# Optimization experiments

Hardware: AMD Instinct MI355X
Metric: run time of the kernel (lower is better)

The kernel has to match this reference:

```python
import jax, jax.numpy as jnp
import numpy as np

COMMISSION_RATIO = 0.0025
INTEREST_RATE = 0.00008
B, N = 4096, 8192


def setup_inputs() -> dict:
    key = jax.random.key(0)
    k1, k2 = jax.random.split(key)
    w = jax.random.uniform(k1, (B, 1, N), dtype=jnp.float32)
    w = w / jnp.sum(w, axis=-1, keepdims=True)  # portfolio weights sum to 1
    # price relatives close to 1 so log(reward) stays finite
    y = 1.0 + 0.02 * jax.random.normal(k2, (B, N, 1), dtype=jnp.float32)
    return {"w": w, "y": y}


def reference(w, y):
    # reward[b] = w[b] @ y[b]  -> [B,1,1]
    reward = jnp.einsum('bin,bnj->bij', w, y)
    # torch .view(B, 1, N) on contiguous [B, N, 1] == transpose here
    close_price = jnp.swapaxes(y, 1, 2)                     # [B,1,N]
    element_reward = w * close_price                        # [B,1,N]
    # interest: only negative elements contribute
    interest = jnp.sum(jnp.minimum(element_reward, 0.0), axis=2,
                       keepdims=True) * INTEREST_RATE       # [B,1,1]
    future_omega = element_reward / reward                  # [B,1,N]
    wt, wt1 = future_omega[:-1], w[1:]
    pure_pc = 1.0 - jnp.sum(jnp.abs(wt - wt1), axis=-1) * COMMISSION_RATIO  # [B-1,1]
    pure_pc = jnp.concatenate(
        [jnp.ones((1, 1), dtype=pure_pc.dtype), pure_pc], axis=0)  # [B,1]
    pure_pc = pure_pc[:, :, None]                           # [B,1,1]
    reward = reward * pure_pc + interest                    # [B,1,1]

    sr_reward = reward - 1.0
    SR = jnp.mean(sr_reward) / jnp.std(sr_reward, ddof=1)   # torch std is unbiased

    # max drawdown: cumprod of per-step changes, running max, relative dip
    pc = reward.reshape(-1)                                 # [B]
    pv = jnp.cumprod(pc)
    running_max = jax.lax.cummax(pv)
    MDD = jnp.max(1.0 - pv / running_max)

    portfolio_value = jnp.prod(reward, axis=0)              # [1,1]
    loss = -jnp.mean(jnp.log(reward))
    return loss, portfolio_value, SR, MDD
```

## Files before the change

### kernel.cpp

```cpp
#include <hip/hip_runtime.h>
#include <math.h>

#define B_DIM 4096
#define N_DIM 8192
#define K_ROWS 16
#define NBLK (B_DIM / K_ROWS)

__constant__ const float kCommission = 0.0025f;
__constant__ const float kInterest   = 8e-05f;

__global__ __launch_bounds__(256) void fused_reward_kernel(const float* __restrict__ w,
                                                           const float* __restrict__ y,
                                                           float* __restrict__ reward_out) {
    const int s    = blockIdx.x * K_ROWS;
    const int tid  = threadIdx.x;
    const int lane = tid & 63, wave = tid >> 6;
    __shared__ float red[2][4][3];

    const int rp = (s == 0) ? 0 : s - 1;
    {
        const float4* wb = (const float4*)(w + (size_t)rp * N_DIM);
        const float4* yb = (const float4*)(y + (size_t)rp * N_DIM);
        float4 wv[8], yv[8];
        #pragma unroll
        for (int j = 0; j < 8; ++j) wv[j] = wb[tid + 256 * j];
        #pragma unroll
        for (int j = 0; j < 8; ++j) yv[j] = yb[tid + 256 * j];
        float d = 0.f;
        float4 ep[8];
        #pragma unroll
        for (int j = 0; j < 8; ++j) {
            float4 ev;
            ev.x = wv[j].x * yv[j].x; ev.y = wv[j].y * yv[j].y;
            ev.z = wv[j].z * yv[j].z; ev.w = wv[j].w * yv[j].w;
            d += (ev.x + ev.y) + (ev.z + ev.w);
            ep[j] = ev;
        }
        (void)d; (void)ep;
    }

    float4 wv[8], yv[8];
    float4 e_prev[8];
    float  inv_dprev;

    {
        const float4* wb = (const float4*)(w + (size_t)rp * N_DIM);
        const float4* yb = (const float4*)(y + (size_t)rp * N_DIM);
        #pragma unroll
        for (int j = 0; j < 8; ++j) wv[j] = wb[tid + 256 * j];
        #pragma unroll
        for (int j = 0; j < 8; ++j) yv[j] = yb[tid + 256 * j];

        float d = 0.f;
        #pragma unroll
        for (int j = 0; j < 8; ++j) {
            float4 ev;
            ev.x = wv[j].x * yv[j].x; ev.y = wv[j].y * yv[j].y;
            ev.z = wv[j].z * yv[j].z; ev.w = wv[j].w * yv[j].w;
            d += (ev.x + ev.y) + (ev.z + ev.w);
            e_prev[j] = ev;
        }

        const float4* wc = (const float4*)(w + (size_t)s * N_DIM);
        const float4* yc = (const float4*)(y + (size_t)s * N_DIM);
        #pragma unroll
        for (int j = 0; j < 8; ++j) wv[j] = wc[tid + 256 * j];
        #pragma unroll
        for (int j = 0; j < 8; ++j) yv[j] = yc[tid + 256 * j];

        #pragma unroll
        for (int off = 32; off; off >>= 1) d += __shfl_down(d, off);
        if (lane == 0) red[0][wave][0] = d;
        __syncthreads();
        inv_dprev = 1.0f / ((red[0][0][0] + red[0][1][0]) + (red[0][2][0] + red[0][3][0]));
    }

    #pragma unroll 1
    for (int k = 0; k < K_ROWS; ++k) {
        const int r = s + k;

        float d = 0.f, it = 0.f, cm = 0.f;
        #pragma unroll
        for (int j = 0; j < 8; ++j) {
            float4 ev;
            ev.x = wv[j].x * yv[j].x; ev.y = wv[j].y * yv[j].y;
            ev.z = wv[j].z * yv[j].z; ev.w = wv[j].w * yv[j].w;
            d  += (ev.x + ev.y) + (ev.z + ev.w);
            it += (fminf(ev.x, 0.f) + fminf(ev.y, 0.f)) +
                  (fminf(ev.z, 0.f) + fminf(ev.w, 0.f));
            cm += (fabsf(fmaf(e_prev[j].x, inv_dprev, -wv[j].x)) +
                   fabsf(fmaf(e_prev[j].y, inv_dprev, -wv[j].y))) +
                  (fabsf(fmaf(e_prev[j].z, inv_dprev, -wv[j].z)) +
                   fabsf(fmaf(e_prev[j].w, inv_dprev, -wv[j].w)));
            e_prev[j] = ev;
        }

        if (k + 1 < K_ROWS) {
            const float4* wn = (const float4*)(w + (size_t)(r + 1) * N_DIM);
            const float4* yn = (const float4*)(y + (size_t)(r + 1) * N_DIM);
            #pragma unroll
            for (int j = 0; j < 8; ++j) wv[j] = wn[tid + 256 * j];
            #pragma unroll
            for (int j = 0; j < 8; ++j) yv[j] = yn[tid + 256 * j];
        }

        #pragma unroll
        for (int off = 32; off; off >>= 1) {
            d  += __shfl_down(d,  off);
            it += __shfl_down(it, off);
            cm += __shfl_down(cm, off);
        }
        const int pb = (k + 1) & 1;
        if (lane == 0) { red[pb][wave][0] = d; red[pb][wave][1] = it; red[pb][wave][2] = cm; }
        __syncthreads();
        const float dot_r = (red[pb][0][0] + red[pb][1][0]) + (red[pb][2][0] + red[pb][3][0]);
        const float int_r = ((red[pb][0][1] + red[pb][1][1]) + (red[pb][2][1] + red[pb][3][1])) * kInterest;
        const float comm  = (red[pb][0][2] + red[pb][1][2]) + (red[pb][2][2] + red[pb][3][2]);
        const float pc = (r == 0) ? 1.0f : fmaf(-comm, kCommission, 1.0f);
        if (tid == 0) reward_out[r] = dot_r * pc + int_r;
        inv_dprev = 1.0f / dot_r;
    }
}

__global__ __launch_bounds__(1024) void finalize_kernel(const float* __restrict__ reward,
                                                        float* __restrict__ out) {
    const int T = 1024, PER = B_DIM / T;
    const int tid = threadIdx.x;
    const int lane = tid & 63, wave = tid >> 6;

    float r[PER], lc[PER];
    float csum = 0.f;
    #pragma unroll
    for (int j = 0; j < PER; ++j) {
        r[j] = reward[tid * PER + j];
        csum += logf(r[j]);
        lc[j] = csum;
    }

    float v = csum;
    #pragma unroll
    for (int off = 1; off < 64; off <<= 1) {
        float t = __shfl_up(v, off);
        if (lane >= off) v += t;
    }
    __shared__ float wsum[16];
    __shared__ float woff[17];
    if (lane == 63) wsum[wave] = v;
    __syncthreads();
    if (tid == 0) {
        float acc = 0.f;
        for (int i = 0; i < 16; ++i) { woff[i] = acc; acc += wsum[i]; }
        woff[16] = acc;
    }
    __syncthreads();
    float ev = __shfl_up(v, 1);
    if (lane == 0) ev = 0.f;
    const float excl = woff[wave] + ev;
    float S[PER];
    #pragma unroll
    for (int j = 0; j < PER; ++j) S[j] = excl + lc[j];
    const float total_logs = woff[16];

    float rm = -INFINITY;
    float cmax[PER];
    #pragma unroll
    for (int j = 0; j < PER; ++j) { rm = fmaxf(rm, S[j]); cmax[j] = rm; }
    float mv = rm;
    #pragma unroll
    for (int off = 1; off < 64; off <<= 1) {
        float t = __shfl_up(mv, off);
        if (lane >= off) mv = fmaxf(mv, t);
    }
    __shared__ float wmax[16];
    __shared__ float wmoff[16];
    if (lane == 63) wmax[wave] = mv;
    __syncthreads();
    if (tid == 0) {
        float acc = -INFINITY;
        for (int i = 0; i < 16; ++i) { wmoff[i] = acc; acc = fmaxf(acc, wmax[i]); }
    }
    __syncthreads();
    float emv = __shfl_up(mv, 1);
    if (lane == 0) emv = -INFINITY;
    const float mexcl = fmaxf(wmoff[wave], emv);

    float ddmax = 0.f;
    #pragma unroll
    for (int j = 0; j < PER; ++j) {
        float M = fmaxf(mexcl, cmax[j]);
        ddmax = fmaxf(ddmax, 1.0f - expf(S[j] - M));
    }
    #pragma unroll
    for (int off = 32; off; off >>= 1) ddmax = fmaxf(ddmax, __shfl_down(ddmax, off));
    __shared__ float wdd[16];
    if (lane == 0) wdd[wave] = ddmax;

    double sr_ = 0.0;
    #pragma unroll
    for (int j = 0; j < PER; ++j) sr_ += (double)r[j];
    #pragma unroll
    for (int off = 32; off; off >>= 1) sr_ += __shfl_down(sr_, off);
    __shared__ double wsr[16];
    if (lane == 0) wsr[wave] = sr_;
    __syncthreads();
    __shared__ double mean_sh;
    if (tid == 0) {
        double sm = 0.0;
        for (int i = 0; i < 16; ++i) sm += wsr[i];
        mean_sh = sm / (double)B_DIM;
    }
    __syncthreads();
    const double mean = mean_sh;
    double sq = 0.0;
    #pragma unroll
    for (int j = 0; j < PER; ++j) { double dd = (double)r[j] - mean; sq += dd * dd; }
    #pragma unroll
    for (int off = 32; off; off >>= 1) sq += __shfl_down(sq, off);
    __shared__ double wsq[16];
    if (lane == 0) wsq[wave] = sq;
    __syncthreads();

    if (tid == 0) {
        double sm = 0.0;
        for (int i = 0; i < 16; ++i) sm += wsq[i];
        double var = sm / (double)(B_DIM - 1);
        double SR = (mean - 1.0) / sqrt(var);
        float mdd = 0.f;
        for (int i = 0; i < 16; ++i) mdd = fmaxf(mdd, wdd[i]);
        out[0] = -total_logs / (float)B_DIM;
        out[1] = expf(total_logs);
        out[2] = (float)SR;
        out[3] = mdd;
    }
}

extern "C" void kernel_launch(void* const* d_in, const int* in_sizes, int n_in,
                              void* d_out, int out_size, void* d_ws, size_t ws_size,
                              hipStream_t stream) {
    const float* w = (const float*)d_in[0];
    const float* y = (const float*)d_in[1];
    float* out = (float*)d_out;
    float* rew = (float*)d_ws;

    fused_reward_kernel<<<NBLK, 256, 0, stream>>>(w, y, rew);
    finalize_kernel<<<1, 1024, 0, stream>>>(rew, out);
}
```

Before: 50.70 us.

## Fuse finalize into reward kernel via last-block ticket and drop redundant preload

Merges the separate single-block finalize kernel into the main reward kernel: each block takes an atomic ticket after writing its rewards, and the last block to finish runs a 256-thread version of the finalize reduction. This removes a second kernel launch and its launch gap. It also deletes a redundant warm-up block that reloaded and recomputed the previous row and threw the result away. The cost is a memset plus an atomic and fence per block, and the finalize now runs with 256 threads instead of 1024.

```diff
diff --git a/kernel.cpp b/kernel.cpp
--- a/kernel.cpp
+++ b/kernel.cpp
@@ -9,41 +9,125 @@
 __constant__ const float kCommission = 0.0025f;
 __constant__ const float kInterest   = 8e-05f;
 
-__global__ __launch_bounds__(256) void fused_reward_kernel(const float* __restrict__ w,
-                                                           const float* __restrict__ y,
-                                                           float* __restrict__ reward_out) {
+__device__ void finalize_256(const float* __restrict__ reward, float* __restrict__ out) {
+    const int PER = 16;
+    const int tid  = threadIdx.x;
+    const int lane = tid & 63, wave = tid >> 6;
+
+    float r[PER], lc[PER];
+    float csum = 0.f;
+    #pragma unroll
+    for (int j = 0; j < PER; ++j) {
+        r[j] = reward[tid * PER + j];
+        csum += logf(r[j]);
+        lc[j] = csum;
+    }
+
+    float v = csum;
+    #pragma unroll
+    for (int off = 1; off < 64; off <<= 1) {
+        float t = __shfl_up(v, off);
+        if (lane >= off) v += t;
+    }
+    __shared__ float wsum[4], woff[5];
+    if (lane == 63) wsum[wave] = v;
+    __syncthreads();
+    if (tid == 0) {
+        float acc = 0.f;
+        for (int i = 0; i < 4; ++i) { woff[i] = acc; acc += wsum[i]; }
+        woff[4] = acc;
+    }
+    __syncthreads();
+    float ev = __shfl_up(v, 1);
+    if (lane == 0) ev = 0.f;
+    const float excl = woff[wave] + ev;
+    float S[PER];
+    #pragma unroll
+    for (int j = 0; j < PER; ++j) S[j] = excl + lc[j];
+    const float total_logs = woff[4];
+
+    float rm = -INFINITY;
+    float cmax[PER];
+    #pragma unroll
+    for (int j = 0; j < PER; ++j) { rm = fmaxf(rm, S[j]); cmax[j] = rm; }
+    float mv = rm;
+    #pragma unroll
+    for (int off = 1; off < 64; off <<= 1) {
+        float t = __shfl_up(mv, off);
+        if (lane >= off) mv = fmaxf(mv, t);
+    }
+    __shared__ float wmax[4], wmoff[4];
+    if (lane == 63) wmax[wave] = mv;
+    __syncthreads();
+    if (tid == 0) {
+        float acc = -INFINITY;
+        for (int i = 0; i < 4; ++i) { wmoff[i] = acc; acc = fmaxf(acc, wmax[i]); }
+    }
+    __syncthreads();
+    float emv = __shfl_up(mv, 1);
+    if (lane == 0) emv = -INFINITY;
+    const float mexcl = fmaxf(wmoff[wave], emv);
+
+    float ddmax = 0.f;
+    #pragma unroll
+    for (int j = 0; j < PER; ++j) {
+        float M = fmaxf(mexcl, cmax[j]);
+        ddmax = fmaxf(ddmax, 1.0f - expf(S[j] - M));
+    }
+    #pragma unroll
+    for (int off = 32; off; off >>= 1) ddmax = fmaxf(ddmax, __shfl_down(ddmax, off));
+    __shared__ float wdd[4];
+    if (lane == 0) wdd[wave] = ddmax;
+
+    double sr_ = 0.0;
+    #pragma unroll
+    for (int j = 0; j < PER; ++j) sr_ += (double)r[j];
+    #pragma unroll
+    for (int off = 32; off; off >>= 1) sr_ += __shfl_down(sr_, off);
+    __shared__ double wsr[4];
+    if (lane == 0) wsr[wave] = sr_;
+    __syncthreads();
+    __shared__ double mean_sh;
+    if (tid == 0) mean_sh = (wsr[0] + wsr[1] + wsr[2] + wsr[3]) / (double)B_DIM;
+    __syncthreads();
+    const double mean = mean_sh;
+    double sq = 0.0;
+    #pragma unroll
+    for (int j = 0; j < PER; ++j) { double dd = (double)r[j] - mean; sq += dd * dd; }
+    #pragma unroll
+    for (int off = 32; off; off >>= 1) sq += __shfl_down(sq, off);
+    __shared__ double wsq[4];
+    if (lane == 0) wsq[wave] = sq;
+    __syncthreads();
+
+    if (tid == 0) {
+        double s = wsq[0] + wsq[1] + wsq[2] + wsq[3];
+        double var = s / (double)(B_DIM - 1);
+        double SR = (mean - 1.0) / sqrt(var);
+        float mdd = fmaxf(fmaxf(wdd[0], wdd[1]), fmaxf(wdd[2], wdd[3]));
+        out[0] = -total_logs / (float)B_DIM;
+        out[1] = expf(total_logs);
+        out[2] = (float)SR;
+        out[3] = mdd;
+    }
+}
+
+__global__ __launch_bounds__(256) void fused_all_kernel(const float* __restrict__ w,
+                                                        const float* __restrict__ y,
+                                                        float* __restrict__ reward_out,
+                                                        int* __restrict__ ticket,
+                                                        float* __restrict__ out) {
     const int s    = blockIdx.x * K_ROWS;
     const int tid  = threadIdx.x;
     const int lane = tid & 63, wave = tid >> 6;
     __shared__ float red[2][4][3];
 
-    const int rp = (s == 0) ? 0 : s - 1;
-    {
-        const float4* wb = (const float4*)(w + (size_t)rp * N_DIM);
-        const float4* yb = (const float4*)(y + (size_t)rp * N_DIM);
-        float4 wv[8], yv[8];
-        #pragma unroll
-        for (int j = 0; j < 8; ++j) wv[j] = wb[tid + 256 * j];
-        #pragma unroll
-        for (int j = 0; j < 8; ++j) yv[j] = yb[tid + 256 * j];
-        float d = 0.f;
-        float4 ep[8];
-        #pragma unroll
-        for (int j = 0; j < 8; ++j) {
-            float4 ev;
-            ev.x = wv[j].x * yv[j].x; ev.y = wv[j].y * yv[j].y;
-            ev.z = wv[j].z * yv[j].z; ev.w = wv[j].w * yv[j].w;
-            d += (ev.x + ev.y) + (ev.z + ev.w);
-            ep[j] = ev;
-        }
-        (void)d; (void)ep;
-    }
-
     float4 wv[8], yv[8];
     float4 e_prev[8];
     float  inv_dprev;
 
     {
+        const int rp = (s == 0) ? 0 : s - 1;
         const float4* wb = (const float4*)(w + (size_t)rp * N_DIM);
         const float4* yb = (const float4*)(y + (size_t)rp * N_DIM);
         #pragma unroll
@@ -120,117 +204,17 @@
         if (tid == 0) reward_out[r] = dot_r * pc + int_r;
         inv_dprev = 1.0f / dot_r;
     }
-}
-
-__global__ __launch_bounds__(1024) void finalize_kernel(const float* __restrict__ reward,
-                                                        float* __restrict__ out) {
-    const int T = 1024, PER = B_DIM / T;
-    const int tid = threadIdx.x;
-    const int lane = tid & 63, wave = tid >> 6;
-
-    float r[PER], lc[PER];
-    float csum = 0.f;
-    #pragma unroll
-    for (int j = 0; j < PER; ++j) {
-        r[j] = reward[tid * PER + j];
-        csum += logf(r[j]);
-        lc[j] = csum;
-    }
-
-    float v = csum;
-    #pragma unroll
-    for (int off = 1; off < 64; off <<= 1) {
-        float t = __shfl_up(v, off);
-        if (lane >= off) v += t;
-    }
-    __shared__ float wsum[16];
-    __shared__ float woff[17];
-    if (lane == 63) wsum[wave] = v;
-    __syncthreads();
-    if (tid == 0) {
-        float acc = 0.f;
-        for (int i = 0; i < 16; ++i) { woff[i] = acc; acc += wsum[i]; }
-        woff[16] = acc;
-    }
-    __syncthreads();
-    float ev = __shfl_up(v, 1);
-    if (lane == 0) ev = 0.f;
-    const float excl = woff[wave] + ev;
-    float S[PER];
-    #pragma unroll
-    for (int j = 0; j < PER; ++j) S[j] = excl + lc[j];
-    const float total_logs = woff[16];
-
-    float rm = -INFINITY;
-    float cmax[PER];
-    #pragma unroll
-    for (int j = 0; j < PER; ++j) { rm = fmaxf(rm, S[j]); cmax[j] = rm; }
-    float mv = rm;
-    #pragma unroll
-    for (int off = 1; off < 64; off <<= 1) {
-        float t = __shfl_up(mv, off);
-        if (lane >= off) mv = fmaxf(mv, t);
-    }
-    __shared__ float wmax[16];
-    __shared__ float wmoff[16];
-    if (lane == 63) wmax[wave] = mv;
-    __syncthreads();
-    if (tid == 0) {
-        float acc = -INFINITY;
-        for (int i = 0; i < 16; ++i) { wmoff[i] = acc; acc = fmaxf(acc, wmax[i]); }
-    }
-    __syncthreads();
-    float emv = __shfl_up(mv, 1);
-    if (lane == 0) emv = -INFINITY;
-    const float mexcl = fmaxf(wmoff[wave], emv);
-
-    float ddmax = 0.f;
-    #pragma unroll
-    for (int j = 0; j < PER; ++j) {
-        float M = fmaxf(mexcl, cmax[j]);
-        ddmax = fmaxf(ddmax, 1.0f - expf(S[j] - M));
-    }
-    #pragma unroll
-    for (int off = 32; off; off >>= 1) ddmax = fmaxf(ddmax, __shfl_down(ddmax, off));
-    __shared__ float wdd[16];
-    if (lane == 0) wdd[wave] = ddmax;
-
-    double sr_ = 0.0;
-    #pragma unroll
-    for (int j = 0; j < PER; ++j) sr_ += (double)r[j];
-    #pragma unroll
-    for (int off = 32; off; off >>= 1) sr_ += __shfl_down(sr_, off);
-    __shared__ double wsr[16];
-    if (lane == 0) wsr[wave] = sr_;
-    __syncthreads();
-    __shared__ double mean_sh;
-    if (tid == 0) {
-        double sm = 0.0;
-        for (int i = 0; i < 16; ++i) sm += wsr[i];
-        mean_sh = sm / (double)B_DIM;
-    }
-    __syncthreads();
-    const double mean = mean_sh;
-    double sq = 0.0;
-    #pragma unroll
-    for (int j = 0; j < PER; ++j) { double dd = (double)r[j] - mean; sq += dd * dd; }
-    #pragma unroll
-    for (int off = 32; off; off >>= 1) sq += __shfl_down(sq, off);
-    __shared__ double wsq[16];
-    if (lane == 0) wsq[wave] = sq;
-    __syncthreads();
-
-    if (tid == 0) {
-        double sm = 0.0;
-        for (int i = 0; i < 16; ++i) sm += wsq[i];
-        double var = sm / (double)(B_DIM - 1);
-        double SR = (mean - 1.0) / sqrt(var);
-        float mdd = 0.f;
-        for (int i = 0; i < 16; ++i) mdd = fmaxf(mdd, wdd[i]);
-        out[0] = -total_logs / (float)B_DIM;
-        out[1] = expf(total_logs);
-        out[2] = (float)SR;
-        out[3] = mdd;
+
+    __shared__ int is_last;
+    if (tid == 0) {
+        __threadfence();
+        int prev = atomicAdd(ticket, 1);
+        is_last = (prev == NBLK - 1) ? 1 : 0;
+    }
+    __syncthreads();
+    if (is_last) {
+        __threadfence();
+        finalize_256(reward_out, out);
     }
 }
 
@@ -240,8 +224,10 @@
     const float* w = (const float*)d_in[0];
     const float* y = (const float*)d_in[1];
     float* out = (float*)d_out;
-    float* rew = (float*)d_ws;
-
-    fused_reward_kernel<<<NBLK, 256, 0, stream>>>(w, y, rew);
-    finalize_kernel<<<1, 1024, 0, stream>>>(rew, out);
+
+    float* rew    = (float*)d_ws;
+    int*   ticket = (int*)((char*)d_ws + B_DIM * sizeof(float));
+
+    hipMemsetAsync(ticket, 0, sizeof(int), stream);
+    fused_all_kernel<<<NBLK, 256, 0, stream>>>(w, y, rew, ticket, out);
 }
```

After: 58.29 us. +15.0%, slower.
